# Kernel tuning notes

Hardware: AMD Instinct MI355X
Metric: run time of the kernel (lower is better)

Reference implementation:

```python
import jax, jax.numpy as jnp
import numpy as np

EPSILON = 1e-15
CUTOFF = 5.0
N_RBF = 16           # num_radial_filters -> RBF dim = 2*16+1 = 33
SCALE = 8            # _quadrature_points_per_atom_scaling


def poly_envelope_5_2(x):
    # e3nn.poly_envelope(5, 2): f'(x) ~ x^5 (1-x)^2, f(0)=1, f(1)=0
    x2 = x * x
    x6 = x2 * x2 * x2
    f = 1.0 - 28.0 * x6 + 48.0 * x6 * x - 21.0 * x6 * x2
    return jnp.where(x < 1.0, f, jnp.zeros_like(x))


def sin_cos_basis(r, n_rbf):
    r = r[..., None]                                  # [A,T,1]
    k = jnp.arange(1, n_rbf + 1, dtype=r.dtype)       # [n_rbf]
    return jnp.sqrt(2.0) * jnp.concatenate(
        [0.1 * jnp.ones_like(r), jnp.sin(k * jnp.pi * r), jnp.cos(k * jnp.pi * r)],
        axis=-1,
    )                                                 # [A,T,2*n_rbf+1]


def spherical_harmonics_l012_norm(d):
    # Real spherical harmonics up to l=2, e3nn m-ordering, normalization='norm'
    # (each l-block has unit norm for unit input directions).
    x, y, z = d[..., 0], d[..., 1], d[..., 2]
    r2 = x * x + y * y + z * z
    s3 = jnp.sqrt(3.0)
    one = jnp.ones_like(x)
    return jnp.stack(
        [
            one,                       # l=0
            y, z, x,                   # l=1 (m=-1,0,1)
            s3 * x * y,                # l=2 m=-2
            s3 * y * z,                # l=2 m=-1
            0.5 * (3.0 * z * z - r2),  # l=2 m=0
            s3 * x * z,                # l=2 m=1
            0.5 * s3 * (x * x - y * y) # l=2 m=2
        ],
        axis=-1,
    )                                  # [A,T,9]


def setup_inputs() -> dict:
    key = jax.random.key(0)
    k1, k2, k3, k4 = jax.random.split(key, 4)
    A, N = 64, 200000
    nuc_pos = 4.0 * jax.random.normal(k1, (A, 3), dtype=jnp.float32)
    grid_coords = 4.0 * jax.random.normal(k2, (N, 3), dtype=jnp.float32)
    weights = jax.random.uniform(k3, (N,), dtype=jnp.float32)
    n = jax.random.uniform(k4, (N,), dtype=jnp.float32)
    atom_mask = jnp.ones((A,), dtype=bool)
    return {"nuc_pos": nuc_pos, "atom_mask": atom_mask,
            "grid_coords": grid_coords, "weights": weights, "n": n}


def reference(nuc_pos, atom_mask, grid_coords, weights, n):
    g = grid_coords / CUTOFF                          # [N,3]
    p = nuc_pos / CUTOFF                              # [A,3]
    diff = p[:, None] - g[None]                       # [A,N,3]
    dist = jnp.linalg.norm(diff, axis=-1)             # [A,N]
    A, N = dist.shape
    T = min(N, SCALE * N // A)                        # static
    idx = jnp.argsort(dist, axis=1)[:, :T]            # [A,T] nearest grid points
    diff = jnp.take_along_axis(diff, idx[:, :, None], axis=1)   # [A,T,3]
    dist = jnp.take_along_axis(dist, idx, axis=1)                # [A,T]
    n_t = n[idx]                                      # [A,T]
    w_t = weights[idx]                                # [A,T]
    rbf = sin_cos_basis(dist, N_RBF) * poly_envelope_5_2(dist)[..., None]  # [A,T,33]
    dirs = diff / (dist[..., None] + EPSILON)         # [A,T,3]
    sh = spherical_harmonics_l012_norm(dirs)          # [A,T,9]
    node_feats = jnp.einsum('atr,ath,at,at->arh', rbf, sh, n_t, w_t)  # [A,33,9]
    return node_feats
```

## Files before the change

### kernel.cpp

```cpp
#include <hip/hip_runtime.h>
#include <hip/hip_fp16.h>


typedef float f32x4 __attribute__((ext_vector_type(4)));
typedef int   i32x4 __attribute__((ext_vector_type(4)));

#define SLICES 32
#define NB1    256
#define NB2    512
#define CLAMP0 4000u
#define CHA    2
#define NCHUNK (SLICES * CHA)
#define PBSTR  304
#define CUT25  0x41C80000u

__device__ __forceinline__ unsigned short tobf(float v) {
  return (unsigned short)((__float_as_uint(v) + 0x8000u) >> 16);
}

__device__ __forceinline__ unsigned pack2h(float a, float b) {
  __half2 h = __floats2half2_rn(a, b);
  return *reinterpret_cast<unsigned*>(&h);
}

__device__ __forceinline__ void mfma_acc(f32x4& d, i32x4 a, i32x4 b) {
  asm("v_mfma_f32_16x16x32_bf16 %0, %1, %2, %0" : "+v"(d) : "v"(a), "v"(b));
}

__global__ __launch_bounds__(256) void enc_hist_store(
    const float* __restrict__ nuc, const float* __restrict__ grid,
    const float* __restrict__ wv, const float* __restrict__ nv, int N,
    unsigned* __restrict__ hists, unsigned* __restrict__ cnt,
    uint4* __restrict__ recs, int scap, unsigned* __restrict__ ghist2) {
  __shared__ unsigned lh[NB1];
  __shared__ unsigned s_cnt;
  int a = blockIdx.x / SLICES, s = blockIdx.x % SLICES;
  int tid = threadIdx.x, lane = tid & 63;
  if (tid < NB1) lh[tid] = 0;
  if (tid == 0) s_cnt = 0;
  {
    const int stripe = NB2 / SLICES;
    if (tid < stripe) ghist2[(size_t)a * NB2 + s * stripe + tid] = 0;
  }
  __syncthreads();

  float px = nuc[3*a+0], py = nuc[3*a+1], pz = nuc[3*a+2];
  uint4* seg = recs + (size_t)blockIdx.x * scap;
  const float4* G4 = (const float4*)grid;
  const float4* W4 = (const float4*)wv;
  const float4* V4 = (const float4*)nv;
  int nq = N >> 2;
  int qper = (nq + SLICES - 1) / SLICES;
  int qlo = s * qper, qhi = min(nq, qlo + qper);

  for (int qi = qlo + tid; qi < qhi; qi += 256) {
    float4 A4 = G4[3*qi], B4 = G4[3*qi+1], C4 = G4[3*qi+2];
    float4 w4 = W4[qi], v4 = V4[qi];
    float xs[4] = {A4.x, A4.w, B4.z, C4.y};
    float ys[4] = {A4.y, B4.x, B4.w, C4.z};
    float zs[4] = {A4.z, B4.y, C4.x, C4.w};
    float nws[4] = {v4.x * w4.x, v4.y * w4.y, v4.z * w4.z, v4.w * w4.w};
    float dxs[4], dys[4], dzs[4];
    unsigned bt[4];
    #pragma unroll
    for (int k = 0; k < 4; ++k) {
      float dx = px - xs[k], dy = py - ys[k], dz = pz - zs[k];
      dxs[k] = dx; dys[k] = dy; dzs[k] = dz;
      float d2 = __fmaf_rn(dx, dx, __fmaf_rn(dy, dy, __fmul_rn(dz, dz)));
      bt[k] = __float_as_uint(d2);
      if (bt[k] < CUT25) {
        int cb = (int)(bt[k] >> 18) - (int)CLAMP0;
        atomicAdd(&lh[cb > 0 ? cb : 0], 1u);
      }
    }
    #pragma unroll
    for (int k = 0; k < 4; ++k) {
      bool sel = bt[k] < CUT25;
      unsigned long long mm = __ballot(sel);
      if (mm) {
        int leader = __ffsll(mm) - 1;
        unsigned base = 0;
        if (lane == leader) base = atomicAdd(&s_cnt, (unsigned)__popcll(mm));
        base = __shfl(base, leader);
        if (sel) {
          unsigned pos = base + (unsigned)__popcll(mm & ((1ull << lane) - 1ull));
          if (pos < (unsigned)scap) {
            uint4 r;
            r.x = bt[k];
            r.y = pack2h(dxs[k], dys[k]);
            r.z = pack2h(dzs[k], 0.f);
            r.w = __float_as_uint(nws[k]);
            seg[pos] = r;
          }
        }
      }
    }
  }
  if (s == SLICES - 1) {
    for (int i = 4*nq + tid; i < N; i += 256) {
      float dx = px - grid[3*i+0], dy = py - grid[3*i+1], dz = pz - grid[3*i+2];
      float d2 = __fmaf_rn(dx, dx, __fmaf_rn(dy, dy, __fmul_rn(dz, dz)));
      unsigned bits = __float_as_uint(d2);
      bool sel = bits < CUT25;
      if (sel) {
        int cb = (int)(bits >> 18) - (int)CLAMP0;
        atomicAdd(&lh[cb > 0 ? cb : 0], 1u);
      }
      unsigned long long mm = __ballot(sel);
      if (mm) {
        int leader = __ffsll(mm) - 1;
        unsigned base = 0;
        if (lane == leader) base = atomicAdd(&s_cnt, (unsigned)__popcll(mm));
        base = __shfl(base, leader);
        if (sel) {
          unsigned pos = base + (unsigned)__popcll(mm & ((1ull << lane) - 1ull));
          if (pos < (unsigned)scap) {
            uint4 r;
            r.x = bits;
            r.y = pack2h(dx, dy);
            r.z = pack2h(dz, 0.f);
            r.w = __float_as_uint(nv[i] * wv[i]);
            seg[pos] = r;
          }
        }
      }
    }
  }
  __syncthreads();
  if (tid < NB1) hists[(size_t)blockIdx.x * NB1 + tid] = lh[tid];
  if (tid == 0) cnt[blockIdx.x] = s_cnt;
}

__global__ __launch_bounds__(256) void enc_fine(
    const unsigned* __restrict__ hists, const unsigned* __restrict__ cnt,
    const uint4* __restrict__ recs, int scap, unsigned T,
    unsigned* __restrict__ b1r, unsigned* __restrict__ r2r,
    unsigned* __restrict__ ghist2) {
  __shared__ unsigned lh[NB1];
  __shared__ unsigned s_bin, s_pre;
  int seg_id = blockIdx.x;
  int a = seg_id / SLICES, s = seg_id % SLICES;
  int tid = threadIdx.x;
  if (tid < NB1) {
    unsigned acc = 0;
    const unsigned* base = hists + (size_t)a * SLICES * NB1 + tid;
    #pragma unroll 8
    for (int t = 0; t < SLICES; ++t) acc += base[(size_t)t * NB1];
    lh[tid] = acc;
  }
  if (tid == 0) { s_bin = NB1 - 1; s_pre = 0; }
  __syncthreads();
  if (tid < 64) {
    int lane = tid, base = 4 * lane;
    unsigned h0 = lh[base], h1 = lh[base+1], h2 = lh[base+2], h3 = lh[base+3];
    unsigned ssum = h0 + h1 + h2 + h3;
    unsigned p = ssum;
    #pragma unroll
    for (int d = 1; d < 64; d <<= 1) {
      unsigned t = __shfl_up(p, d);
      if (lane >= d) p += t;
    }
    unsigned excl = p - ssum;
    if (excl < T && T <= p) {
      unsigned cum = excl;
      unsigned hh[4] = {h0, h1, h2, h3};
      #pragma unroll
      for (int k = 0; k < 4; ++k) {
        if (cum + hh[k] >= T) { s_bin = (unsigned)(base + k); s_pre = cum; break; }
        cum += hh[k];
      }
    }
  }
  __syncthreads();
  unsigned b1c = s_bin;
  if (s == 0 && tid == 0) { b1r[a] = s_bin; r2r[a] = T - s_pre; }

  unsigned tb1 = b1c + CLAMP0;
  int total = min((int)cnt[seg_id], scap);
  const unsigned* segb = (const unsigned*)(recs + (size_t)seg_id * scap);
  unsigned* gh2 = ghist2 + (size_t)a * NB2;
  for (int i = tid; i < total; i += 256) {
    unsigned bits = segb[4 * i];
    unsigned cb = bits >> 18;
    bool match = b1c ? (cb == tb1) : (cb <= CLAMP0);
    if (match) atomicAdd(&gh2[(bits >> 9) & (NB2 - 1)], 1u);
  }
}

__global__ __launch_bounds__(256, 4) void enc_accum(
    const unsigned* __restrict__ b1r, const unsigned* __restrict__ r2r,
    const unsigned* __restrict__ ghist2, const unsigned* __restrict__ cnt,
    const uint4* __restrict__ recs, int scap, float* __restrict__ pb) {
  __shared__ __align__(16) unsigned short lds[4][4608];
  __shared__ unsigned lh2[NB2];
  __shared__ unsigned s_bin2;
  int seg_id = blockIdx.x / CHA, c = blockIdx.x % CHA;
  int a = seg_id / SLICES;
  int tid = threadIdx.x, lane = tid & 63, w = tid >> 6;
  unsigned short* SB = &lds[w][0];

  {
    i32x4 z = {0, 0, 0, 0};
    i32x4* zp = (i32x4*)SB;
    #pragma unroll
    for (int t = 0; t < 9; ++t) zp[lane + t * 64] = z;
  }
  {
    const unsigned* gh2 = ghist2 + (size_t)a * NB2;
    lh2[tid] = gh2[tid];
    lh2[tid + 256] = gh2[tid + 256];
  }
  if (tid == 0) s_bin2 = NB2 - 1;
  __syncthreads();
  unsigned R = r2r[a];
  if (tid < 64) {
    int lane2 = tid, base = 8 * lane2;
    unsigned hh[8], ssum = 0;
    #pragma unroll
    for (int k = 0; k < 8; ++k) { hh[k] = lh2[base + k]; ssum += hh[k]; }
    unsigned p = ssum;
    #pragma unroll
    for (int d = 1; d < 64; d <<= 1) {
      unsigned t = __shfl_up(p, d);
      if (lane2 >= d) p += t;
    }
    unsigned excl = p - ssum;
    if (excl < R && R <= p) {
      unsigned cum = excl;
      #pragma unroll
      for (int k = 0; k < 8; ++k) {
        if (cum + hh[k] >= R) { s_bin2 = (unsigned)(base + k); break; }
        cum += hh[k];
      }
    }
  }
  __syncthreads();
  unsigned thr = ((b1r[a] + CLAMP0) << 9) | s_bin2;

  int total = min((int)cnt[seg_id], scap);
  const uint4* lst = recs + (size_t)seg_id * scap;

  f32x4 acc0 = {0,0,0,0}, acc1 = {0,0,0,0}, acc2 = {0,0,0,0};
  int m = lane & 15, q = lane >> 4;
  const float SQRT2 = 1.41421356237309515f;
  const float PIF   = 3.14159265358979323846f;
  const float S3    = 1.73205080756887729f;

  for (int jb = c * 256 + w * 64; jb < total; jb += CHA * 256) {
    int j = jb + lane;
    bool valid = j < total;
    uint4 pr;
    if (valid) pr = lst[j]; else pr.x = 0xFFFFFFFFu;
    bool live = valid && ((pr.x >> 9) <= thr);
    if (live) {
      float d2 = __uint_as_float(pr.x);
      __half2 hxy = *reinterpret_cast<const __half2*>(&pr.y);
      __half2 hz2 = *reinterpret_cast<const __half2*>(&pr.z);
      float dx = __low2float(hxy), dy = __high2float(hxy), dz = __low2float(hz2);
      float nw = __uint_as_float(pr.w);
#if __has_builtin(__builtin_amdgcn_sqrtf)
      float rn = __builtin_amdgcn_sqrtf(d2) * 0.2f;
#else
      float rn = sqrtf(d2) * 0.2f;
#endif
      float x2 = rn * rn;
      float x6 = x2 * x2 * x2;
      float e  = __fmaf_rn(x6, __fmaf_rn(-21.f, x2, __fmaf_rn(48.f, rn, -28.f)), 1.f);
      float f  = SQRT2 * e;
#if __has_builtin(__builtin_amdgcn_rcpf)
      float inv = 0.2f * __builtin_amdgcn_rcpf(rn + 1e-15f);
#else
      float inv = 0.2f / (rn + 1e-15f);
#endif
      float X = dx * inv, Y = dy * inv, Z = dz * inv;
      float r2 = __fmaf_rn(X, X, __fmaf_rn(Y, Y, Z * Z));
      SB[3456 + 0*72 + lane] = tobf(nw);
      SB[3456 + 1*72 + lane] = tobf(nw * Y);
      SB[3456 + 2*72 + lane] = tobf(nw * Z);
      SB[3456 + 3*72 + lane] = tobf(nw * X);
      SB[3456 + 4*72 + lane] = tobf(nw * S3 * X * Y);
      SB[3456 + 5*72 + lane] = tobf(nw * S3 * Y * Z);
      SB[3456 + 6*72 + lane] = tobf(nw * 0.5f * __fmaf_rn(3.f, Z * Z, -r2));
      SB[3456 + 7*72 + lane] = tobf(nw * S3 * X * Z);
      SB[3456 + 8*72 + lane] = tobf(nw * 0.5f * S3 * (X * X - Y * Y));
      float s1, c1;
      __sincosf(PIF * rn, &s1, &c1);
      SB[0 * 72 + lane]  = tobf(0.1f * f);
      float sk = s1, ck = c1;
      SB[1 * 72 + lane]  = tobf(f * sk);
      SB[17 * 72 + lane] = tobf(f * ck);
      #pragma unroll
      for (int k = 2; k <= 16; ++k) {
        float sn = __fmaf_rn(sk, c1, ck * s1);
        float cn = __fmaf_rn(ck, c1, -(sk * s1));
        sk = sn; ck = cn;
        SB[k * 72 + lane]        = tobf(f * sk);
        SB[(16 + k) * 72 + lane] = tobf(f * ck);
      }
    } else {
      #pragma unroll
      for (int h = 0; h < 9; ++h) SB[3456 + h * 72 + lane] = 0;
    }
    #pragma unroll
    for (int g = 0; g < 2; ++g) {
      int cb = 8 * q + 32 * g;
      i32x4 bf = *(const i32x4*)&SB[3456 + m * 72 + cb];
      i32x4 a0 = *(const i32x4*)&SB[(0  + m) * 72 + cb];
      mfma_acc(acc0, a0, bf);
      i32x4 a1 = *(const i32x4*)&SB[(16 + m) * 72 + cb];
      mfma_acc(acc1, a1, bf);
      i32x4 a2 = *(const i32x4*)&SB[(32 + m) * 72 + cb];
      mfma_acc(acc2, a2, bf);
    }
  }
  asm volatile("s_nop 7\n\ts_nop 7" : "+v"(acc0), "+v"(acc1), "+v"(acc2));

  float* redw = (float*)&lds[w][0];
  if (m < 9) {
    #pragma unroll
    for (int t = 0; t < 4; ++t) {
      int row = 4 * q + t;
      redw[(row +  0) * 9 + m] = acc0[t];
      redw[(row + 16) * 9 + m] = acc1[t];
      if (row + 32 < 33) redw[(row + 32) * 9 + m] = acc2[t];
    }
  }
  __syncthreads();
  float* pbb = pb + (size_t)blockIdx.x * PBSTR;
  for (int v = tid; v < 297; v += 256) {
    float s0 = ((const float*)&lds[0][0])[v] + ((const float*)&lds[1][0])[v];
    float s1 = ((const float*)&lds[2][0])[v] + ((const float*)&lds[3][0])[v];
    pbb[v] = s0 + s1;
  }
}

__global__ __launch_bounds__(256) void enc_reduce(
    const float* __restrict__ pb, float* __restrict__ out, int nout) {
  int idx = blockIdx.x * 256 + threadIdx.x;
  if (idx >= nout) return;
  int a = idx / 297, v = idx - a * 297;
  const float* p = pb + (size_t)a * NCHUNK * PBSTR + v;
  float s = 0.f;
  #pragma unroll 8
  for (int k = 0; k < NCHUNK; ++k) s += p[(size_t)k * PBSTR];
  out[idx] = s;
}

extern "C" void kernel_launch(void* const* d_in, const int* in_sizes, int n_in,
                              void* d_out, int out_size, void* d_ws, size_t ws_size,
                              hipStream_t stream) {
  const float* nuc  = (const float*)d_in[0];
  const float* grid = (const float*)d_in[2];
  const float* wts  = (const float*)d_in[3];
  const float* nn   = (const float*)d_in[4];
  int A = in_sizes[0] / 3;
  int N = in_sizes[2] / 3;
  long long t8 = (8LL * (long long)N) / (long long)A;
  unsigned T = (unsigned)(t8 < (long long)N ? t8 : (long long)N);

  unsigned* ws     = (unsigned*)d_ws;
  unsigned* cnt    = ws;
  unsigned* b1r    = cnt + A * SLICES;
  unsigned* r2r    = b1r + A;
  unsigned* hists  = r2r + A;
  unsigned* ghist2 = hists + (size_t)A * SLICES * NB1;
  float*    pb     = (float*)(ghist2 + (size_t)A * NB2);
  uint4*    recs   = (uint4*)(pb + (size_t)A * SLICES * CHA * PBSTR);

  int nq   = N >> 2;
  int qper = (nq + SLICES - 1) / SLICES;
  int SCAP = qper * 4 + 4;
  {
    long long head  = (long long)(((unsigned*)recs) - ws);
    long long avail = (long long)(ws_size / 4) - head;
    long long need  = 4LL * SCAP * A * SLICES;
    if (avail > 0 && need > avail) SCAP = (int)(avail / (4LL * A * SLICES));
  }
  float* out = (float*)d_out;
  int nout = A * 297;

  enc_hist_store<<<A * SLICES,         256, 0, stream>>>(nuc, grid, wts, nn, N, hists,
                                                         cnt, recs, SCAP, ghist2);
  enc_fine      <<<A * SLICES,         256, 0, stream>>>(hists, cnt, recs, SCAP, T,
                                                         b1r, r2r, ghist2);
  enc_accum     <<<A * SLICES * CHA,   256, 0, stream>>>(b1r, r2r, ghist2, cnt,
                                                         recs, SCAP, pb);
  enc_reduce    <<<(nout + 255) / 256, 256, 0, stream>>>(pb, out, nout);
}
```

Measured before the change: 64.83 us.

## Split candidate records into key and payload arrays, hoist per-atom scans into kernels

Candidate records are stored as a separate 4-byte key array plus an 8-byte payload, with the n*w product packed as fp16 next to dz, instead of one 16-byte record. The fine-histogram pass now reads only the keys, which cuts its traffic. The per-atom histogram scans that every block used to repeat are moved into small dedicated kernels (scan1, scan2). Accumulation LDS shrinks to 49 rows, which allows higher occupancy (launch bound 5). In exchange there are two extra kernel launches, and storing n*w as fp16 loses precision.

```diff
diff --git a/kernel.cpp b/kernel.cpp
--- a/kernel.cpp
+++ b/kernel.cpp
@@ -13,6 +13,8 @@
 #define NCHUNK (SLICES * CHA)
 #define PBSTR  304
 #define CUT25  0x41C80000u
+#define WROWS  49
+#define BBASE  (33 * 72)
 
 __device__ __forceinline__ unsigned short tobf(float v) {
   return (unsigned short)((__float_as_uint(v) + 0x8000u) >> 16);
@@ -31,7 +33,8 @@
     const float* __restrict__ nuc, const float* __restrict__ grid,
     const float* __restrict__ wv, const float* __restrict__ nv, int N,
     unsigned* __restrict__ hists, unsigned* __restrict__ cnt,
-    uint4* __restrict__ recs, int scap, unsigned* __restrict__ ghist2) {
+    unsigned* __restrict__ bitsArr, uint2* __restrict__ pay, int scap,
+    unsigned* __restrict__ ghist2) {
   __shared__ unsigned lh[NB1];
   __shared__ unsigned s_cnt;
   int a = blockIdx.x / SLICES, s = blockIdx.x % SLICES;
@@ -45,7 +48,8 @@
   __syncthreads();
 
   float px = nuc[3*a+0], py = nuc[3*a+1], pz = nuc[3*a+2];
-  uint4* seg = recs + (size_t)blockIdx.x * scap;
+  unsigned* segb = bitsArr + (size_t)blockIdx.x * scap;
+  uint2*    segp = pay     + (size_t)blockIdx.x * scap;
   const float4* G4 = (const float4*)grid;
   const float4* W4 = (const float4*)wv;
   const float4* V4 = (const float4*)nv;
@@ -85,12 +89,8 @@
         if (sel) {
           unsigned pos = base + (unsigned)__popcll(mm & ((1ull << lane) - 1ull));
           if (pos < (unsigned)scap) {
-            uint4 r;
-            r.x = bt[k];
-            r.y = pack2h(dxs[k], dys[k]);
-            r.z = pack2h(dzs[k], 0.f);
-            r.w = __float_as_uint(nws[k]);
-            seg[pos] = r;
+            segb[pos] = bt[k];
+            segp[pos] = make_uint2(pack2h(dxs[k], dys[k]), pack2h(dzs[k], nws[k]));
           }
         }
       }
@@ -115,12 +115,8 @@
         if (sel) {
           unsigned pos = base + (unsigned)__popcll(mm & ((1ull << lane) - 1ull));
           if (pos < (unsigned)scap) {
-            uint4 r;
-            r.x = bits;
-            r.y = pack2h(dx, dy);
-            r.z = pack2h(dz, 0.f);
-            r.w = __float_as_uint(nv[i] * wv[i]);
-            seg[pos] = r;
+            segb[pos] = bits;
+            segp[pos] = make_uint2(pack2h(dx, dy), pack2h(dz, nv[i] * wv[i]));
           }
         }
       }
@@ -131,16 +127,12 @@
   if (tid == 0) cnt[blockIdx.x] = s_cnt;
 }
 
-__global__ __launch_bounds__(256) void enc_fine(
-    const unsigned* __restrict__ hists, const unsigned* __restrict__ cnt,
-    const uint4* __restrict__ recs, int scap, unsigned T,
-    unsigned* __restrict__ b1r, unsigned* __restrict__ r2r,
-    unsigned* __restrict__ ghist2) {
+__global__ __launch_bounds__(256) void enc_scan1(
+    const unsigned* __restrict__ hists, unsigned T,
+    unsigned* __restrict__ b1r, unsigned* __restrict__ r2r) {
   __shared__ unsigned lh[NB1];
   __shared__ unsigned s_bin, s_pre;
-  int seg_id = blockIdx.x;
-  int a = seg_id / SLICES, s = seg_id % SLICES;
-  int tid = threadIdx.x;
+  int a = blockIdx.x, tid = threadIdx.x;
   if (tid < NB1) {
     unsigned acc = 0;
     const unsigned* base = hists + (size_t)a * SLICES * NB1 + tid;
@@ -172,49 +164,42 @@
     }
   }
   __syncthreads();
-  unsigned b1c = s_bin;
-  if (s == 0 && tid == 0) { b1r[a] = s_bin; r2r[a] = T - s_pre; }
-
+  if (tid == 0) { b1r[a] = s_bin; r2r[a] = T - s_pre; }
+}
+
+__global__ __launch_bounds__(256) void enc_fine(
+    const unsigned* __restrict__ b1r, const unsigned* __restrict__ cnt,
+    const unsigned* __restrict__ bitsArr, int scap,
+    unsigned* __restrict__ ghist2) {
+  int seg_id = blockIdx.x;
+  int a = seg_id / SLICES;
+  unsigned b1c = b1r[a];
   unsigned tb1 = b1c + CLAMP0;
   int total = min((int)cnt[seg_id], scap);
-  const unsigned* segb = (const unsigned*)(recs + (size_t)seg_id * scap);
+  const unsigned* segb = bitsArr + (size_t)seg_id * scap;
   unsigned* gh2 = ghist2 + (size_t)a * NB2;
-  for (int i = tid; i < total; i += 256) {
-    unsigned bits = segb[4 * i];
+  for (int i = threadIdx.x; i < total; i += 256) {
+    unsigned bits = segb[i];
     unsigned cb = bits >> 18;
     bool match = b1c ? (cb == tb1) : (cb <= CLAMP0);
     if (match) atomicAdd(&gh2[(bits >> 9) & (NB2 - 1)], 1u);
   }
 }
 
-__global__ __launch_bounds__(256, 4) void enc_accum(
-    const unsigned* __restrict__ b1r, const unsigned* __restrict__ r2r,
-    const unsigned* __restrict__ ghist2, const unsigned* __restrict__ cnt,
-    const uint4* __restrict__ recs, int scap, float* __restrict__ pb) {
-  __shared__ __align__(16) unsigned short lds[4][4608];
+__global__ __launch_bounds__(256) void enc_scan2(
+    const unsigned* __restrict__ ghist2, const unsigned* __restrict__ b1r,
+    const unsigned* __restrict__ r2r, unsigned* __restrict__ thr) {
   __shared__ unsigned lh2[NB2];
   __shared__ unsigned s_bin2;
-  int seg_id = blockIdx.x / CHA, c = blockIdx.x % CHA;
-  int a = seg_id / SLICES;
-  int tid = threadIdx.x, lane = tid & 63, w = tid >> 6;
-  unsigned short* SB = &lds[w][0];
-
-  {
-    i32x4 z = {0, 0, 0, 0};
-    i32x4* zp = (i32x4*)SB;
-    #pragma unroll
-    for (int t = 0; t < 9; ++t) zp[lane + t * 64] = z;
-  }
-  {
-    const unsigned* gh2 = ghist2 + (size_t)a * NB2;
-    lh2[tid] = gh2[tid];
-    lh2[tid + 256] = gh2[tid + 256];
-  }
+  int a = blockIdx.x, tid = threadIdx.x;
+  const unsigned* gh2 = ghist2 + (size_t)a * NB2;
+  lh2[tid] = gh2[tid];
+  lh2[tid + 256] = gh2[tid + 256];
   if (tid == 0) s_bin2 = NB2 - 1;
   __syncthreads();
   unsigned R = r2r[a];
   if (tid < 64) {
-    int lane2 = tid, base = 8 * lane2;
+    int lane = tid, base = 8 * lane;
     unsigned hh[8], ssum = 0;
     #pragma unroll
     for (int k = 0; k < 8; ++k) { hh[k] = lh2[base + k]; ssum += hh[k]; }
@@ -222,7 +207,7 @@
     #pragma unroll
     for (int d = 1; d < 64; d <<= 1) {
       unsigned t = __shfl_up(p, d);
-      if (lane2 >= d) p += t;
+      if (lane >= d) p += t;
     }
     unsigned excl = p - ssum;
     if (excl < R && R <= p) {
@@ -235,10 +220,33 @@
     }
   }
   __syncthreads();
-  unsigned thr = ((b1r[a] + CLAMP0) << 9) | s_bin2;
-
+  if (tid == 0) thr[a] = ((b1r[a] + CLAMP0) << 9) | s_bin2;
+}
+
+__global__ __launch_bounds__(256, 5) void enc_accum(
+    const unsigned* __restrict__ thrv, const unsigned* __restrict__ cnt,
+    const unsigned* __restrict__ bitsArr, const uint2* __restrict__ pay,
+    int scap, float* __restrict__ pb) {
+  __shared__ __align__(16) unsigned short lds[4][WROWS * 72];
+  int seg_id = blockIdx.x / CHA, c = blockIdx.x % CHA;
+  int a = seg_id / SLICES;
+  int tid = threadIdx.x, lane = tid & 63, w = tid >> 6;
+  unsigned short* SB = &lds[w][0];
+
+  {
+    i32x4 z = {0, 0, 0, 0};
+    i32x4* zp = (i32x4*)SB;
+    #pragma unroll
+    for (int t = 0; t < 7; ++t) {
+      int idx = lane + t * 64;
+      if (idx < (WROWS * 72) / 8) zp[idx] = z;
+    }
+  }
+
+  unsigned thr = thrv[a];
   int total = min((int)cnt[seg_id], scap);
-  const uint4* lst = recs + (size_t)seg_id * scap;
+  const unsigned* lstb = bitsArr + (size_t)seg_id * scap;
+  const uint2*    lstp = pay     + (size_t)seg_id * scap;
 
   f32x4 acc0 = {0,0,0,0}, acc1 = {0,0,0,0}, acc2 = {0,0,0,0};
   int m = lane & 15, q = lane >> 4;
@@ -249,15 +257,16 @@
   for (int jb = c * 256 + w * 64; jb < total; jb += CHA * 256) {
     int j = jb + lane;
     bool valid = j < total;
-    uint4 pr;
-    if (valid) pr = lst[j]; else pr.x = 0xFFFFFFFFu;
-    bool live = valid && ((pr.x >> 9) <= thr);
+    unsigned bits = valid ? lstb[j] : 0xFFFFFFFFu;
+    uint2 pr = make_uint2(0u, 0u);
+    if (valid) pr = lstp[j];
+    bool live = valid && ((bits >> 9) <= thr);
     if (live) {
-      float d2 = __uint_as_float(pr.x);
-      __half2 hxy = *reinterpret_cast<const __half2*>(&pr.y);
-      __half2 hz2 = *reinterpret_cast<const __half2*>(&pr.z);
-      float dx = __low2float(hxy), dy = __high2float(hxy), dz = __low2float(hz2);
-      float nw = __uint_as_float(pr.w);
+      float d2 = __uint_as_float(bits);
+      __half2 hxy = *reinterpret_cast<const __half2*>(&pr.x);
+      __half2 hzn = *reinterpret_cast<const __half2*>(&pr.y);
+      float dx = __low2float(hxy), dy = __high2float(hxy);
+      float dz = __low2float(hzn), nw = __high2float(hzn);
 #if __has_builtin(__builtin_amdgcn_sqrtf)
       float rn = __builtin_amdgcn_sqrtf(d2) * 0.2f;
 #else
@@ -274,15 +283,15 @@
 #endif
       float X = dx * inv, Y = dy * inv, Z = dz * inv;
       float r2 = __fmaf_rn(X, X, __fmaf_rn(Y, Y, Z * Z));
-      SB[3456 + 0*72 + lane] = tobf(nw);
-      SB[3456 + 1*72 + lane] = tobf(nw * Y);
-      SB[3456 + 2*72 + lane] = tobf(nw * Z);
-      SB[3456 + 3*72 + lane] = tobf(nw * X);
-      SB[3456 + 4*72 + lane] = tobf(nw * S3 * X * Y);
-      SB[3456 + 5*72 + lane] = tobf(nw * S3 * Y * Z);
-      SB[3456 + 6*72 + lane] = tobf(nw * 0.5f * __fmaf_rn(3.f, Z * Z, -r2));
-      SB[3456 + 7*72 + lane] = tobf(nw * S3 * X * Z);
-      SB[3456 + 8*72 + lane] = tobf(nw * 0.5f * S3 * (X * X - Y * Y));
+      SB[BBASE + 0*72 + lane] = tobf(nw);
+      SB[BBASE + 1*72 + lane] = tobf(nw * Y);
+      SB[BBASE + 2*72 + lane] = tobf(nw * Z);
+      SB[BBASE + 3*72 + lane] = tobf(nw * X);
+      SB[BBASE + 4*72 + lane] = tobf(nw * S3 * X * Y);
+      SB[BBASE + 5*72 + lane] = tobf(nw * S3 * Y * Z);
+      SB[BBASE + 6*72 + lane] = tobf(nw * 0.5f * __fmaf_rn(3.f, Z * Z, -r2));
+      SB[BBASE + 7*72 + lane] = tobf(nw * S3 * X * Z);
+      SB[BBASE + 8*72 + lane] = tobf(nw * 0.5f * S3 * (X * X - Y * Y));
       float s1, c1;
       __sincosf(PIF * rn, &s1, &c1);
       SB[0 * 72 + lane]  = tobf(0.1f * f);
@@ -299,12 +308,12 @@
       }
     } else {
       #pragma unroll
-      for (int h = 0; h < 9; ++h) SB[3456 + h * 72 + lane] = 0;
+      for (int h = 0; h < 9; ++h) SB[BBASE + h * 72 + lane] = 0;
     }
     #pragma unroll
     for (int g = 0; g < 2; ++g) {
       int cb = 8 * q + 32 * g;
-      i32x4 bf = *(const i32x4*)&SB[3456 + m * 72 + cb];
+      i32x4 bf = *(const i32x4*)&SB[BBASE + m * 72 + cb];
       i32x4 a0 = *(const i32x4*)&SB[(0  + m) * 72 + cb];
       mfma_acc(acc0, a0, bf);
       i32x4 a1 = *(const i32x4*)&SB[(16 + m) * 72 + cb];
@@ -358,32 +367,35 @@
   long long t8 = (8LL * (long long)N) / (long long)A;
   unsigned T = (unsigned)(t8 < (long long)N ? t8 : (long long)N);
 
-  unsigned* ws     = (unsigned*)d_ws;
-  unsigned* cnt    = ws;
-  unsigned* b1r    = cnt + A * SLICES;
-  unsigned* r2r    = b1r + A;
-  unsigned* hists  = r2r + A;
-  unsigned* ghist2 = hists + (size_t)A * SLICES * NB1;
-  float*    pb     = (float*)(ghist2 + (size_t)A * NB2);
-  uint4*    recs   = (uint4*)(pb + (size_t)A * SLICES * CHA * PBSTR);
+  unsigned* ws      = (unsigned*)d_ws;
+  unsigned* cnt     = ws;
+  unsigned* b1r     = cnt + A * SLICES;
+  unsigned* r2r     = b1r + A;
+  unsigned* thr     = r2r + A;
+  unsigned* hists   = thr + A;
+  unsigned* ghist2  = hists + (size_t)A * SLICES * NB1;
+  float*    pb      = (float*)(ghist2 + (size_t)A * NB2);
+  unsigned* bitsArr = (unsigned*)(pb + (size_t)A * SLICES * CHA * PBSTR);
 
   int nq   = N >> 2;
   int qper = (nq + SLICES - 1) / SLICES;
   int SCAP = qper * 4 + 4;
   {
-    long long head  = (long long)(((unsigned*)recs) - ws);
+    long long head  = (long long)(bitsArr - ws);
     long long avail = (long long)(ws_size / 4) - head;
-    long long need  = 4LL * SCAP * A * SLICES;
-    if (avail > 0 && need > avail) SCAP = (int)(avail / (4LL * A * SLICES));
-  }
+    long long need  = 3LL * SCAP * A * SLICES;
+    if (avail > 0 && need > avail) SCAP = (int)(avail / (3LL * A * SLICES));
+    SCAP &= ~1;
+  }
+  uint2* pay = (uint2*)(bitsArr + (size_t)A * SLICES * SCAP);
   float* out = (float*)d_out;
   int nout = A * 297;
 
   enc_hist_store<<<A * SLICES,         256, 0, stream>>>(nuc, grid, wts, nn, N, hists,
-                                                         cnt, recs, SCAP, ghist2);
-  enc_fine      <<<A * SLICES,         256, 0, stream>>>(hists, cnt, recs, SCAP, T,
-                                                         b1r, r2r, ghist2);
-  enc_accum     <<<A * SLICES * CHA,   256, 0, stream>>>(b1r, r2r, ghist2, cnt,
-                                                         recs, SCAP, pb);
+                                                         cnt, bitsArr, pay, SCAP, ghist2);
+  enc_scan1     <<<A,                  256, 0, stream>>>(hists, T, b1r, r2r);
+  enc_fine      <<<A * SLICES,         256, 0, stream>>>(b1r, cnt, bitsArr, SCAP, ghist2);
+  enc_scan2     <<<A,                  256, 0, stream>>>(ghist2, b1r, r2r, thr);
+  enc_accum     <<<A * SLICES * CHA,   256, 0, stream>>>(thr, cnt, bitsArr, pay, SCAP, pb);
   enc_reduce    <<<(nout + 255) / 256, 256, 0, stream>>>(pb, out, nout);
 }
```

Result: no change. 63.81 us (-1.6%).
